# Kernel tuning notes

Hardware: AMD Instinct MI355X
Metric: run time of the kernel (lower is better)

## Reference

```python
import jax, jax.numpy as jnp
import numpy as np

B, T, E, H = 256, 256, 384, 64

def setup_inputs() -> dict:
    key = jax.random.key(0)
    ks = jax.random.split(key, 4)
    s = 1.0 / np.sqrt(E)
    return {
        "x":  jax.random.normal(ks[0], (B, T, E), dtype=jnp.float32),
        "Wq": jax.random.normal(ks[1], (E, H), dtype=jnp.float32) * s,
        "bq": jnp.zeros((H,), dtype=jnp.float32),
        "Wk": jax.random.normal(ks[2], (E, H), dtype=jnp.float32) * s,
        "bk": jnp.zeros((H,), dtype=jnp.float32),
        "Wv": jax.random.normal(ks[3], (E, H), dtype=jnp.float32) * s,
        "bv": jnp.zeros((H,), dtype=jnp.float32),
    }

def reference(x, Wq, bq, Wk, bk, Wv, bv):
    # QKV projections: [B,T,E] @ [E,H] -> [B,T,H]
    q = x @ Wq + bq
    k = x @ Wk + bk
    v = x @ Wv + bv
    # attention scores (NOTE: original has no 1/sqrt(d) scaling)
    wei = jnp.einsum('bth,bsh->bts', q, k)  # [B,T,T]
    causal = jnp.tril(jnp.ones((T, T), dtype=bool))
    wei = jnp.where(causal, wei, -jnp.inf)
    wei = jax.nn.softmax(wei, axis=-1)
    # dropout is identity in eval mode
    out = jnp.einsum('bts,bsh->bth', wei, v)  # [B,T,H]
    return out
```

## Files before the change

### kernel.cpp

```cpp
#include <hip/hip_runtime.h>
#include <math.h>

#define Bb 256
#define Tt 256
#define Ee 384
#define Hh 64

typedef __attribute__((ext_vector_type(8))) short bf16x8;
typedef __attribute__((ext_vector_type(4))) float f32x4;

__device__ inline short f2bf(float f) {
    unsigned u = __float_as_uint(f);
    u += 0x7FFFu + ((u >> 16) & 1);
    return (short)(u >> 16);
}
__device__ inline float bf2f(short s) {
    return __uint_as_float(((unsigned)(unsigned short)s) << 16);
}

#define MFMA16(a, b, c) __builtin_amdgcn_mfma_f32_16x16x32_bf16((a), (b), (c), 0, 0, 0)

#define WLO_OFF 147456

#define BB0 65536
#define K_HI 0
#define K_LO 32768
#define VF   65536
#define QH   98304
#define QL   116736
#define PBASE 98304
#define SMEM_BYTES 135168

__global__ __launch_bounds__(256) void prep_w(
    const float* __restrict__ Wq, const float* __restrict__ Wk,
    const float* __restrict__ Wv, unsigned char* __restrict__ wsp)
{
    int u = blockIdx.x * 256 + threadIdx.x;
    if (u >= 9216) return;
    int frag = u >> 6;
    int lu   = u & 63;
    int ec   = frag / 12, tct = frag - ec * 12;
    int koct = lu >> 4, n = lu & 15;
    int col  = tct * 16 + n;
    const float* Wm = (col < 64) ? Wq : ((col < 128) ? Wk : Wv);
    int c = col & 63;
    bf16x8 hi8, lo8;
    #pragma unroll
    for (int j = 0; j < 8; ++j) {
        float v = Wm[(ec * 32 + koct * 8 + j) * 64 + c];
        short h = f2bf(v);
        hi8[j] = h;
        lo8[j] = f2bf(v - bf2f(h));
    }
    *reinterpret_cast<bf16x8*>(wsp + frag * 1024 + lu * 16) = hi8;
    *reinterpret_cast<bf16x8*>(wsp + WLO_OFF + frag * 1024 + lu * 16) = lo8;
}

__global__ __launch_bounds__(1024) void head_fused(
    const float* __restrict__ x,
    const float* __restrict__ bq, const float* __restrict__ bk,
    const float* __restrict__ bv,
    const unsigned char* __restrict__ wsp,
    float* __restrict__ out)
{
    __shared__ __align__(16) unsigned char smem[SMEM_BYTES];

    const int b    = blockIdx.x;
    const int tid  = threadIdx.x;
    const int w    = tid >> 6;
    const int lane = tid & 63;
    const int quad = lane >> 4;
    const int nl   = lane & 15;
    const int ri   = w >> 2;
    const int cj   = w & 3;

    f32x4 acc[4][3];
    #pragma unroll
    for (int i = 0; i < 4; ++i)
        #pragma unroll
        for (int j = 0; j < 3; ++j) acc[i][j] = (f32x4){0,0,0,0};

    const float4* x4 = reinterpret_cast<const float4*>(x + (size_t)b * Tt * Ee);

    const int At  = ((tid >> 6) << 4) + (tid & 15);
    const int Ako = (tid >> 4) & 3;
    const float4* xsrc = x4 + At * 96 + Ako * 2;

    auto bgld = [&](int ecn) {
        if (w < 12) {
            int p = ecn & 1;
            const unsigned char* ghi = wsp + (size_t)(ecn * 12 + w) * 1024 + (size_t)lane * 16;
            const unsigned char* glo = ghi + WLO_OFF;
            __builtin_amdgcn_global_load_lds(
                (const __attribute__((address_space(1))) unsigned*)ghi,
                (__attribute__((address_space(3))) unsigned*)(smem + BB0 + p * 24576 + w * 1024),
                16, 0, 0);
            __builtin_amdgcn_global_load_lds(
                (const __attribute__((address_space(1))) unsigned*)glo,
                (__attribute__((address_space(3))) unsigned*)(smem + BB0 + p * 24576 + 12288 + w * 1024),
                16, 0, 0);
        }
    };

    bgld(0);
    float4 pa0 = xsrc[0], pa1 = xsrc[1];
    {
        float v[8] = {pa0.x, pa0.y, pa0.z, pa0.w, pa1.x, pa1.y, pa1.z, pa1.w};
        bf16x8 hi8, lo8;
        #pragma unroll
        for (int j = 0; j < 8; ++j) {
            short h = f2bf(v[j]);
            hi8[j] = h;
            lo8[j] = f2bf(v[j] - bf2f(h));
        }
        *reinterpret_cast<bf16x8*>(smem + tid * 16) = hi8;
        *reinterpret_cast<bf16x8*>(smem + 16384 + tid * 16) = lo8;
    }
    pa0 = xsrc[8]; pa1 = xsrc[9];

    for (int ec = 0; ec < 12; ++ec) {
        __syncthreads();
        if (ec < 11) bgld(ec + 1);
        if (ec < 11) {
            float v[8] = {pa0.x, pa0.y, pa0.z, pa0.w, pa1.x, pa1.y, pa1.z, pa1.w};
            bf16x8 hi8, lo8;
            #pragma unroll
            for (int j = 0; j < 8; ++j) {
                short h = f2bf(v[j]);
                hi8[j] = h;
                lo8[j] = f2bf(v[j] - bf2f(h));
            }
            int nb = (1 - (ec & 1)) * 32768;
            *reinterpret_cast<bf16x8*>(smem + nb + tid * 16) = hi8;
            *reinterpret_cast<bf16x8*>(smem + nb + 16384 + tid * 16) = lo8;
        }
        if (ec < 10) { pa0 = xsrc[(ec + 2) * 8]; pa1 = xsrc[(ec + 2) * 8 + 1]; }

        const int ab = (ec & 1) * 32768;
        const int bb = BB0 + (ec & 1) * 24576;
        bf16x8 bh[3], bl[3];
        #pragma unroll
        for (int ct = 0; ct < 3; ++ct) {
            int o = bb + (cj * 3 + ct) * 1024 + lane * 16;
            bh[ct] = *reinterpret_cast<bf16x8*>(smem + o);
            bl[ct] = *reinterpret_cast<bf16x8*>(smem + o + 12288);
        }
        #pragma unroll
        for (int rt = 0; rt < 4; ++rt) {
            int ao = ab + (4 * ri + rt) * 1024 + lane * 16;
            bf16x8 ah = *reinterpret_cast<bf16x8*>(smem + ao);
            bf16x8 al = *reinterpret_cast<bf16x8*>(smem + ao + 16384);
            #pragma unroll
            for (int ct = 0; ct < 3; ++ct) {
                acc[rt][ct] = MFMA16(ah, bh[ct], acc[rt][ct]);
                acc[rt][ct] = MFMA16(al, bh[ct], acc[rt][ct]);
                acc[rt][ct] = MFMA16(ah, bl[ct], acc[rt][ct]);
            }
        }
    }
    __syncthreads();

    #pragma unroll
    for (int ct = 0; ct < 3; ++ct) {
        int col = (cj * 3 + ct) * 16 + nl;
        float bias = (col < 64) ? bq[col] : (col < 128 ? bk[col - 64] : bv[col - 128]);
        #pragma unroll
        for (int rt = 0; rt < 4; ++rt)
            #pragma unroll
            for (int r = 0; r < 4; ++r) acc[rt][ct][r] += bias;
    }

    #pragma unroll
    for (int ct = 0; ct < 3; ++ct) {
        int col = (cj * 3 + ct) * 16 + nl;
        #pragma unroll
        for (int rt = 0; rt < 4; ++rt) {
            #pragma unroll
            for (int r = 0; r < 4; ++r) {
                float val = acc[rt][ct][r];
                int s = ri * 64 + rt * 16 + quad * 4 + r;
                if (col >= 64 && col < 128) {
                    int h = col - 64;
                    int addr = ((s >> 4) * 2 + (h >> 5)) * 1024
                             + ((((h & 31) >> 3) * 16 + (s & 15)) * 8 + (h & 7)) * 2;
                    short hi = f2bf(val);
                    short lo = f2bf(val - bf2f(hi));
                    *reinterpret_cast<short*>(smem + K_HI + addr) = hi;
                    *reinterpret_cast<short*>(smem + K_LO + addr) = lo;
                } else if (col >= 128) {
                    int h = col - 128, sl = s & 31;
                    int addr = ((s >> 5) * 4 + (h >> 4)) * 1024
                             + (((sl >> 3) * 16 + (h & 15)) * 8 + (sl & 7)) * 2;
                    *reinterpret_cast<short*>(smem + VF + addr) = f2bf(val);
                }
            }
        }
    }

    auto writeQhalf = [&]() {
        #pragma unroll
        for (int ct = 0; ct < 3; ++ct) {
            int col = (cj * 3 + ct) * 16 + nl;
            if (col < 64) {
                #pragma unroll
                for (int rt = 0; rt < 4; ++rt) {
                    #pragma unroll
                    for (int r = 0; r < 4; ++r) {
                        float val = acc[rt][ct][r];
                        int s = ri * 64 + rt * 16 + quad * 4 + r;
                        int rloc = s & 127;
                        short hi = f2bf(val);
                        short lo = f2bf(val - bf2f(hi));
                        *reinterpret_cast<short*>(smem + QH + (rloc * 72 + col) * 2) = hi;
                        *reinterpret_cast<short*>(smem + QL + (rloc * 72 + col) * 2) = lo;
                    }
                }
            }
        }
    };
    bf16x8 qh0, qh1, ql0, ql1;
    auto readQ = [&]() {
        int rloc = (16 * w + nl) & 127;
        int base = rloc * 144;
        qh0 = *reinterpret_cast<bf16x8*>(smem + QH + base + quad * 16);
        qh1 = *reinterpret_cast<bf16x8*>(smem + QH + base + 64 + quad * 16);
        ql0 = *reinterpret_cast<bf16x8*>(smem + QL + base + quad * 16);
        ql1 = *reinterpret_cast<bf16x8*>(smem + QL + base + 64 + quad * 16);
    };

    if (ri < 2) writeQhalf();
    __syncthreads();
    if (w < 8) readQ();
    __syncthreads();
    if (ri >= 2) writeQhalf();
    __syncthreads();
    if (w >= 8) readQ();
    __syncthreads();

    f32x4 oacc[4];
    #pragma unroll
    for (int i = 0; i < 4; ++i) oacc[i] = (f32x4){0,0,0,0};
    float lsum = 0.f;
    const int t0 = w * 16;
    unsigned char* pb = smem + PBASE + w * 1344;
    const int npairs = (w >> 1) + 1;

    for (int p = 0; p < npairs; ++p) {
        #pragma unroll
        for (int hf = 0; hf < 2; ++hf) {
            int st = 2 * p + hf;
            f32x4 s0 = (f32x4){0,0,0,0}, s1 = (f32x4){0,0,0,0};
            int kb = st * 2048 + lane * 16;
            bf16x8 kh0 = *reinterpret_cast<bf16x8*>(smem + K_HI + kb);
            bf16x8 kh1 = *reinterpret_cast<bf16x8*>(smem + K_HI + kb + 1024);
            bf16x8 kl0 = *reinterpret_cast<bf16x8*>(smem + K_LO + kb);
            bf16x8 kl1 = *reinterpret_cast<bf16x8*>(smem + K_LO + kb + 1024);
            s0 = MFMA16(qh0, kh0, s0);
            s1 = MFMA16(qh1, kh1, s1);
            s0 = MFMA16(ql0, kh0, s0);
            s1 = MFMA16(ql1, kh1, s1);
            s0 = MFMA16(qh0, kl0, s0);
            s1 = MFMA16(qh1, kl1, s1);
            int sg = st * 16 + nl;
            #pragma unroll
            for (int r = 0; r < 4; ++r) {
                int tg = t0 + quad * 4 + r;
                float sv = s0[r] + s1[r];
                float pv = (sg <= tg) ? __expf(sv) : 0.f;
                *reinterpret_cast<short*>(pb + ((quad * 4 + r) * 40 + hf * 16 + nl) * 2) = f2bf(pv);
            }
        }
        asm volatile("s_waitcnt lgkmcnt(0)" ::: "memory");
        bf16x8 pa = *reinterpret_cast<bf16x8*>(pb + (nl * 40 + quad * 8) * 2);
        float ls = 0.f;
        #pragma unroll
        for (int j = 0; j < 8; ++j) ls += bf2f(pa[j]);
        ls += __shfl_xor(ls, 16);
        ls += __shfl_xor(ls, 32);
        lsum += ls;
        int vb = p * 4096 + lane * 16;
        #pragma unroll
        for (int nt = 0; nt < 4; ++nt) {
            bf16x8 vf = *reinterpret_cast<bf16x8*>(smem + VF + vb + nt * 1024);
            oacc[nt] = MFMA16(pa, vf, oacc[nt]);
        }
    }

    float* lb_ = reinterpret_cast<float*>(pb + 1280);
    if (lane < 16) lb_[lane] = lsum;
    asm volatile("s_waitcnt lgkmcnt(0)" ::: "memory");
    float* ob = out + (size_t)b * Tt * Hh + (size_t)t0 * Hh;
    #pragma unroll
    for (int r = 0; r < 4; ++r) {
        float inv = 1.0f / lb_[quad * 4 + r];
        #pragma unroll
        for (int nt = 0; nt < 4; ++nt)
            ob[(quad * 4 + r) * 64 + nt * 16 + nl] = oacc[nt][r] * inv;
    }
}

extern "C" void kernel_launch(void* const* d_in, const int* in_sizes, int n_in,
                              void* d_out, int out_size, void* d_ws, size_t ws_size,
                              hipStream_t stream) {
    const float* x  = (const float*)d_in[0];
    const float* Wq = (const float*)d_in[1];
    const float* bq = (const float*)d_in[2];
    const float* Wk = (const float*)d_in[3];
    const float* bk = (const float*)d_in[4];
    const float* Wv = (const float*)d_in[5];
    const float* bv = (const float*)d_in[6];
    float* out = (float*)d_out;
    unsigned char* wsp = (unsigned char*)d_ws;
    hipLaunchKernelGGL(prep_w, dim3(36), dim3(256), 0, stream, Wq, Wk, Wv, wsp);
    hipLaunchKernelGGL(head_fused, dim3(Bb), dim3(1024), 0, stream,
                       x, bq, bk, bv, wsp, out);
}
```

Before: 183.3 us.

## Warp-specialize x staging onto spare waves and use packed bf16 conversion

The x tile loading and hi/lo bf16 split is moved from all 16 waves onto the 4 waves that do not issue weight DMA loads. Each of those threads now loads a full 128-byte row chunk with no register prefetch into the next iteration. The split uses the hardware v_cvt_pk_bf16_f32 instruction instead of manual rounding. This lightens the per-iteration work on the MMA-heavy waves but puts all x staging latency on four waves, and the load is no longer prefetched one step ahead.

Measured after the change: 186.3 us. No clear change (+1.6%).

```diff
diff --git a/kernel.cpp b/kernel.cpp
--- a/kernel.cpp
+++ b/kernel.cpp
@@ -8,6 +8,7 @@
 
 typedef __attribute__((ext_vector_type(8))) short bf16x8;
 typedef __attribute__((ext_vector_type(4))) float f32x4;
+typedef __attribute__((ext_vector_type(4))) unsigned int u32x4;
 
 __device__ inline short f2bf(float f) {
     unsigned u = __float_as_uint(f);
@@ -16,6 +17,11 @@
 }
 __device__ inline float bf2f(short s) {
     return __uint_as_float(((unsigned)(unsigned short)s) << 16);
+}
+__device__ inline unsigned cvt_pk_bf16(float a, float b) {
+    unsigned r;
+    asm("v_cvt_pk_bf16_f32 %0, %1, %2" : "=v"(r) : "v"(a), "v"(b));
+    return r;
 }
 
 #define MFMA16(a, b, c) __builtin_amdgcn_mfma_f32_16x16x32_bf16((a), (b), (c), 0, 0, 0)
@@ -82,10 +88,6 @@
 
     const float4* x4 = reinterpret_cast<const float4*>(x + (size_t)b * Tt * Ee);
 
-    const int At  = ((tid >> 6) << 4) + (tid & 15);
-    const int Ako = (tid >> 4) & 3;
-    const float4* xsrc = x4 + At * 96 + Ako * 2;
-
     auto bgld = [&](int ecn) {
         if (w < 12) {
             int p = ecn & 1;
@@ -102,39 +104,50 @@
         }
     };
 
+    const int pt = tid & 255;
+    const float4* xp = x4 + pt * 96;
+    unsigned char* adst = smem + (pt >> 4) * 1024 + (pt & 15) * 16;
+
+    auto stageA = [&](int ecsrc, int nb) {
+        float4 px[8];
+        const float4* xr_ = xp + ecsrc * 8;
+        #pragma unroll
+        for (int j = 0; j < 8; ++j) px[j] = xr_[j];
+        #pragma unroll
+        for (int ko = 0; ko < 4; ++ko) {
+            float v0 = px[2*ko+0].x, v1 = px[2*ko+0].y,
+                  v2 = px[2*ko+0].z, v3 = px[2*ko+0].w,
+                  v4 = px[2*ko+1].x, v5 = px[2*ko+1].y,
+                  v6 = px[2*ko+1].z, v7 = px[2*ko+1].w;
+            unsigned h0 = cvt_pk_bf16(v0, v1);
+            unsigned h1 = cvt_pk_bf16(v2, v3);
+            unsigned h2 = cvt_pk_bf16(v4, v5);
+            unsigned h3 = cvt_pk_bf16(v6, v7);
+            unsigned l0 = cvt_pk_bf16(v0 - __uint_as_float(h0 << 16),
+                                      v1 - __uint_as_float(h0 & 0xFFFF0000u));
+            unsigned l1 = cvt_pk_bf16(v2 - __uint_as_float(h1 << 16),
+                                      v3 - __uint_as_float(h1 & 0xFFFF0000u));
+            unsigned l2 = cvt_pk_bf16(v4 - __uint_as_float(h2 << 16),
+                                      v5 - __uint_as_float(h2 & 0xFFFF0000u));
+            unsigned l3 = cvt_pk_bf16(v6 - __uint_as_float(h3 << 16),
+                                      v7 - __uint_as_float(h3 & 0xFFFF0000u));
+            u32x4 hv = {h0, h1, h2, h3};
+            u32x4 lv = {l0, l1, l2, l3};
+            *reinterpret_cast<u32x4*>(adst + nb + ko * 256) = hv;
+            *reinterpret_cast<u32x4*>(adst + nb + 16384 + ko * 256) = lv;
+        }
+    };
+
     bgld(0);
-    float4 pa0 = xsrc[0], pa1 = xsrc[1];
-    {
-        float v[8] = {pa0.x, pa0.y, pa0.z, pa0.w, pa1.x, pa1.y, pa1.z, pa1.w};
-        bf16x8 hi8, lo8;
-        #pragma unroll
-        for (int j = 0; j < 8; ++j) {
-            short h = f2bf(v[j]);
-            hi8[j] = h;
-            lo8[j] = f2bf(v[j] - bf2f(h));
-        }
-        *reinterpret_cast<bf16x8*>(smem + tid * 16) = hi8;
-        *reinterpret_cast<bf16x8*>(smem + 16384 + tid * 16) = lo8;
-    }
-    pa0 = xsrc[8]; pa1 = xsrc[9];
+    if (w >= 12) stageA(0, 0);
 
     for (int ec = 0; ec < 12; ++ec) {
         __syncthreads();
-        if (ec < 11) bgld(ec + 1);
-        if (ec < 11) {
-            float v[8] = {pa0.x, pa0.y, pa0.z, pa0.w, pa1.x, pa1.y, pa1.z, pa1.w};
-            bf16x8 hi8, lo8;
-            #pragma unroll
-            for (int j = 0; j < 8; ++j) {
-                short h = f2bf(v[j]);
-                hi8[j] = h;
-                lo8[j] = f2bf(v[j] - bf2f(h));
-            }
-            int nb = (1 - (ec & 1)) * 32768;
-            *reinterpret_cast<bf16x8*>(smem + nb + tid * 16) = hi8;
-            *reinterpret_cast<bf16x8*>(smem + nb + 16384 + tid * 16) = lo8;
-        }
-        if (ec < 10) { pa0 = xsrc[(ec + 2) * 8]; pa1 = xsrc[(ec + 2) * 8 + 1]; }
+        if (w < 12) {
+            if (ec < 11) bgld(ec + 1);
+        } else {
+            if (ec < 11) stageA(ec + 1, (1 - (ec & 1)) * 32768);
+        }
 
         const int ab = (ec & 1) * 32768;
         const int bb = BB0 + (ec & 1) * 24576;
@@ -305,8 +318,8 @@
     const float* x  = (const float*)d_in[0];
     const float* Wq = (const float*)d_in[1];
     const float* bq = (const float*)d_in[2];
+    const float* bk = (const float*)d_in[4];
     const float* Wk = (const float*)d_in[3];
-    const float* bk = (const float*)d_in[4];
     const float* Wv = (const float*)d_in[5];
     const float* bv = (const float*)d_in[6];
     float* out = (float*)d_out;
```
